# Performance work log

Hardware: AMD Instinct MI355X
Metric: run time of the kernel (lower is better)

Reference implementation:

```python
import jax, jax.numpy as jnp
import numpy as np

B, U, V, E, D, L4 = 64, 1024, 1024, 512, 640, 4 * 640


def setup_inputs() -> dict:
    key = jax.random.key(0)
    ks = jax.random.split(key, 9)
    return {
        "targets": jax.random.randint(ks[0], (B, U), 0, V),
        "target_lens": jax.random.randint(ks[1], (B,), 1, U + 1),
        "embed": jax.random.normal(ks[2], (V, E), dtype=jnp.float32) * 0.02,
        "W0": jax.random.normal(ks[3], (E, L4), dtype=jnp.float32) * 0.04,
        "U0": jax.random.normal(ks[4], (D, L4), dtype=jnp.float32) * 0.04,
        "b0": jnp.zeros((L4,), dtype=jnp.float32),
        "W1": jax.random.normal(ks[5], (D, L4), dtype=jnp.float32) * 0.04,
        "U1": jax.random.normal(ks[6], (D, L4), dtype=jnp.float32) * 0.04,
        "b1": jnp.zeros((L4,), dtype=jnp.float32),
    }


def _masked_lstm(x, mask, W, Uw, b):
    """Keras-semantics masked LSTM (i,f,g,o gate order). x:[B,T,in], mask:[B,T].
    Masked steps carry state/output forward (Keras RNN mask behavior)."""
    d = Uw.shape[0]
    xz = jnp.einsum('bti,ig->btg', x, W) + b  # precompute input projection [B,T,4D]

    def step(carry, inp):
        h, c = carry
        z_t, m = inp  # [B,4D], [B]
        z = z_t + h @ Uw
        i, f, g, o = jnp.split(z, 4, axis=-1)
        i = jax.nn.sigmoid(i)
        f = jax.nn.sigmoid(f)
        g = jnp.tanh(g)
        o = jax.nn.sigmoid(o)
        c_new = f * c + i * g
        h_new = o * jnp.tanh(c_new)
        m = m[:, None]
        h2 = jnp.where(m, h_new, h)
        c2 = jnp.where(m, c_new, c)
        return (h2, c2), h2

    h0 = jnp.zeros((x.shape[0], d), dtype=x.dtype)
    (_, _), ys = jax.lax.scan(step, (h0, h0), (xz.transpose(1, 0, 2), mask.T))
    return ys.transpose(1, 0, 2)  # [B,T,D]


def reference(targets, target_lens, embed, W0, U0, b0, W1, U1, b1):
    x = embed[targets]  # [B,U,E]
    mask = jnp.arange(targets.shape[1])[None, :] < target_lens[:, None]  # [B,U]
    x = _masked_lstm(x, mask, W0, U0, b0)
    x = _masked_lstm(x, mask, W1, U1, b1)
    return x
```

## Files before the change

kernel.cpp:

```cpp
#include <hip/hip_runtime.h>
#include <math.h>

#define B_   64
#define U_   1024
#define E_   512
#define D_   640
#define L4_  2560
#define TC   64
#define NCH  16
#define NBLK 160
#define SUBQ (NBLK / 8)

template <int MODE>
__global__ __launch_bounds__(256) void gemm_kernel(
    const float* __restrict__ A,
    const int*   __restrict__ targets,
    const float* __restrict__ Wm,
    const float* __restrict__ bias,
    float* __restrict__ xz,
    int K, int t0)
{
    const int tid = threadIdx.x;
    const int m0 = blockIdx.x * 128;
    const int n0 = blockIdx.y * 128;

    __shared__ float As[8][132];
    __shared__ float Bs[8][132];

    float acc[8][8];
#pragma unroll
    for (int i = 0; i < 8; ++i)
#pragma unroll
        for (int j = 0; j < 8; ++j) acc[i][j] = 0.f;

    const float* a_ptr;
    int a_ml = 0, a_kq = 0, a_k = 0;
    if (MODE == 0) {
        a_ml = tid & 127;
        a_kq = (tid >> 7) * 4;
        int m  = m0 + a_ml;
        int b  = m & 63;
        int tl = m >> 6;
        int idx = targets[b * U_ + t0 + tl];
        a_ptr = A + (size_t)idx * E_ + a_kq;
    } else {
        a_k  = tid >> 5;
        a_ml = (tid & 31) * 4;
        int m  = m0 + a_ml;
        int b  = m & 63;
        int tl = m >> 6;
        a_ptr = A + (size_t)tl * (D_ * 64) + (size_t)a_k * 64 + b;
    }
    const int b_k  = tid >> 5;
    const int b_n4 = (tid & 31) * 4;

    const int tx = tid & 15;
    const int ty = tid >> 4;

    for (int k0 = 0; k0 < K; k0 += 8) {
        if (MODE == 0) {
            float4 av = *(const float4*)(a_ptr + k0);
            As[a_kq + 0][a_ml] = av.x;
            As[a_kq + 1][a_ml] = av.y;
            As[a_kq + 2][a_ml] = av.z;
            As[a_kq + 3][a_ml] = av.w;
        } else {
            float4 av = *(const float4*)(a_ptr + (size_t)k0 * 64);
            *(float4*)&As[a_k][a_ml] = av;
        }
        {
            float4 bv = *(const float4*)(Wm + (size_t)(k0 + b_k) * L4_ + n0 + b_n4);
            *(float4*)&Bs[b_k][b_n4] = bv;
        }
        __syncthreads();

#pragma unroll
        for (int k = 0; k < 8; ++k) {
            float af[8], bf[8];
            *(float4*)&af[0] = *(const float4*)&As[k][ty * 8];
            *(float4*)&af[4] = *(const float4*)&As[k][ty * 8 + 4];
            *(float4*)&bf[0] = *(const float4*)&Bs[k][tx * 8];
            *(float4*)&bf[4] = *(const float4*)&Bs[k][tx * 8 + 4];
#pragma unroll
            for (int i = 0; i < 8; ++i)
#pragma unroll
                for (int j = 0; j < 8; ++j) acc[i][j] += af[i] * bf[j];
        }
        __syncthreads();
    }

#pragma unroll
    for (int i = 0; i < 8; ++i) {
        int m  = m0 + ty * 8 + i;
        int tl = m >> 6;
        int b  = m & 63;
        float* outp = xz + (size_t)tl * (L4_ * 64) + b;
#pragma unroll
        for (int j = 0; j < 8; ++j) {
            int n = n0 + tx * 8 + j;
            outp[(size_t)n * 64] = acc[i][j] + bias[n];
        }
    }
}

__global__ __launch_bounds__(256) void prep_up_kernel(
    const float* __restrict__ U0w, const float* __restrict__ U1w,
    float* __restrict__ Up0, float* __restrict__ Up1)
{
    const int k = blockIdx.x;
    const float* Uw = blockIdx.y ? U1w : U0w;
    float*       Up = blockIdx.y ? Up1 : Up0;
    for (int d = threadIdx.x; d < D_; d += 256) {
        const int g  = d >> 2;
        const int dd = d & 3;
#pragma unroll
        for (int gate = 0; gate < 4; ++gate) {
            float v = Uw[(size_t)k * L4_ + gate * 640 + d];
            Up[((size_t)g * 640 + k) * 16 + dd * 4 + gate] = v;
        }
    }
}

__device__ __forceinline__ void stg_llc(float* p, float v) {
    __hip_atomic_store(p, v, __ATOMIC_RELAXED, __HIP_MEMORY_SCOPE_AGENT);
}

__device__ __forceinline__ void grid_barrier(unsigned* bar, unsigned done)
{
    asm volatile("s_waitcnt vmcnt(0)" ::: "memory");
    __syncthreads();
    if (threadIdx.x == 0) {
        unsigned* sub    = bar + ((blockIdx.x & 7) << 5);
        unsigned* master = bar + (8 << 5);
        unsigned a = __hip_atomic_fetch_add(sub, 1u, __ATOMIC_RELAXED, __HIP_MEMORY_SCOPE_AGENT);
        if (a == done * SUBQ - 1u)
            __hip_atomic_fetch_add(master, 1u, __ATOMIC_RELAXED, __HIP_MEMORY_SCOPE_AGENT);
        const unsigned tgt = done * 8u;
        while (__hip_atomic_load(master, __ATOMIC_RELAXED, __HIP_MEMORY_SCOPE_AGENT) < tgt)
            __builtin_amdgcn_s_sleep(1);
    }
    __syncthreads();
}

__global__ __launch_bounds__(512) void lstm_seq_kernel(
    const float* __restrict__ xz,
    const float* __restrict__ Upg,
    const float* __restrict__ hinit,
    float* __restrict__ c_st,
    const int* __restrict__ lens,
    float* __restrict__ hc_out,
    int t0,
    unsigned* __restrict__ bar,
    unsigned bar_base)
{
    const int tid  = threadIdx.x;
    const int d0   = blockIdx.x * 4;
    const int ks   = tid >> 6;
    const int kbeg = ks * 80;
    const int lane   = tid & 63;
    const int n_grp  = lane >> 4;
    const int n_base = n_grp * 4;
    const int b0     = (lane & 15) * 4;

    __shared__ float U_lds[640 * 16];
    __shared__ float red[128][64];

    {
        const float4* upg = (const float4*)(Upg + (size_t)blockIdx.x * (640 * 16));
        float4* udst = (float4*)U_lds;
#pragma unroll
        for (int it = 0; it < 5; ++it)
            udst[it * 512 + tid] = upg[it * 512 + tid];
    }

    const bool epi = tid < 256;
    const int ed = d0 + ((tid >> 6) & 3);
    const int eb = tid & 63;
    float c_reg = 0.f;
    int   len_b = 0;
    if (epi) {
        c_reg = c_st[ed * 64 + eb];
        len_b = lens[eb];
    }

    __syncthreads();

    float acc[16];
    float HA[16], HB[16], HC[16];
    float UA[16], UB[16], UC[16];

#define HLOAD(HH)                                                           \
    _Pragma("unroll")                                                       \
    for (int j = 0; j < 4; ++j)                                             \
        *(float4*)&HH[j * 4] = *(const float4*)(hrun + j * 64);             \
    hrun += 256;

#define ULOAD(UU)                                                           \
    _Pragma("unroll")                                                       \
    for (int j = 0; j < 4; ++j)                                             \
        *(float4*)&UU[j * 4] = *(const float4*)(urun + j * 16);             \
    urun += 64;

#define FMAG(HH, UU)                                                        \
    _Pragma("unroll")                                                       \
    for (int j = 0; j < 4; ++j)                                             \
        _Pragma("unroll")                                                   \
        for (int i = 0; i < 4; ++i)                                         \
            _Pragma("unroll")                                               \
            for (int q = 0; q < 4; ++q)                                     \
                acc[i * 4 + q] += UU[j * 4 + i] * HH[j * 4 + q];

#pragma unroll 1
    for (int tl = 0; tl < TC; ++tl) {
        const int t = t0 + tl;
        const float* hprev = (tl == 0) ? hinit
                           : hc_out + (size_t)(tl - 1) * (D_ * 64);
        float*       hcur  = hc_out + (size_t)tl * (D_ * 64);

        float xzv[4];
        float hp_epi = 0.f;
        if (epi) {
            const float* xzp = xz + (size_t)tl * (L4_ * 64) + eb;
#pragma unroll
            for (int g = 0; g < 4; ++g)
                xzv[g] = xzp[(size_t)(ed + 640 * g) * 64];
            hp_epi = hprev[ed * 64 + eb];
        }

#pragma unroll
        for (int i = 0; i < 16; ++i) acc[i] = 0.f;

        const float* hrun = hprev + (size_t)kbeg * 64 + b0;
        const float* urun = &U_lds[(size_t)kbeg * 16 + n_base];

        HLOAD(HA) ULOAD(UA)
        HLOAD(HB) ULOAD(UB)
        HLOAD(HC) ULOAD(UC)
#pragma unroll 1
        for (int t3 = 0; t3 < 5; ++t3) {
            FMAG(HA, UA) HLOAD(HA) ULOAD(UA)
            FMAG(HB, UB) HLOAD(HB) ULOAD(UB)
            FMAG(HC, UC) HLOAD(HC) ULOAD(UC)
        }
        FMAG(HA, UA) HLOAD(HA) ULOAD(UA)
        FMAG(HB, UB) HLOAD(HB) ULOAD(UB)
        FMAG(HC, UC)
        FMAG(HA, UA)
        FMAG(HB, UB)

        {
            const int colw = b0 ^ (n_grp << 2);
#pragma unroll
            for (int i = 0; i < 4; ++i)
                *(float4*)&red[((n_base + i) << 3) | ks][colw] = *(float4*)&acc[i * 4];
        }
        __syncthreads();

        if (epi) {
            const int dd = (tid >> 6) & 3;
            const int colr = eb ^ (dd << 2);
            float z[4];
#pragma unroll
            for (int g = 0; g < 4; ++g) {
                const int r = ((dd * 4 + g) << 3);
                float s = 0.f;
#pragma unroll
                for (int kk = 0; kk < 8; ++kk) s += red[r + kk][colr];
                z[g] = s + xzv[g];
            }
            float ig = 1.f / (1.f + __expf(-z[0]));
            float fg = 1.f / (1.f + __expf(-z[1]));
            float gg = tanhf(z[2]);
            float og = 1.f / (1.f + __expf(-z[3]));
            float c_new = fg * c_reg + ig * gg;
            float h_new = og * tanhf(c_new);
            bool msk = t < len_b;
            float h_out = msk ? h_new : hp_epi;
            c_reg = msk ? c_new : c_reg;
            stg_llc(hcur + ed * 64 + eb, h_out);
        }

        if (tl != TC - 1)
            grid_barrier(bar, bar_base + (unsigned)tl + 1u);
    }
    if (epi) c_st[ed * 64 + eb] = c_reg;
#undef HLOAD
#undef ULOAD
#undef FMAG
}

__global__ __launch_bounds__(256) void transpose_kernel(
    const float* __restrict__ h1c, float* __restrict__ out, int t0)
{
    const int tl   = blockIdx.x;
    const int dblk = blockIdx.y;
    __shared__ float tile[64][65];

    const int r  = threadIdx.x >> 2;
    const int cq = threadIdx.x & 3;

    const float* src = h1c + (size_t)tl * (D_ * 64) + (size_t)(dblk * 64 + r) * 64 + cq * 16;
#pragma unroll
    for (int j = 0; j < 4; ++j) {
        float4 v = *(const float4*)(src + j * 4);
        tile[r][cq * 16 + j * 4 + 0] = v.x;
        tile[r][cq * 16 + j * 4 + 1] = v.y;
        tile[r][cq * 16 + j * 4 + 2] = v.z;
        tile[r][cq * 16 + j * 4 + 3] = v.w;
    }
    __syncthreads();

    float* dst = out + (size_t)r * (U_ * D_) + (size_t)(t0 + tl) * D_ + dblk * 64 + cq * 16;
#pragma unroll
    for (int j = 0; j < 4; ++j) {
        float4 w;
        w.x = tile[cq * 16 + j * 4 + 0][r];
        w.y = tile[cq * 16 + j * 4 + 1][r];
        w.z = tile[cq * 16 + j * 4 + 2][r];
        w.w = tile[cq * 16 + j * 4 + 3][r];
        *(float4*)(dst + j * 4) = w;
    }
}

extern "C" void kernel_launch(void* const* d_in, const int* in_sizes, int n_in,
                              void* d_out, int out_size, void* d_ws, size_t ws_size,
                              hipStream_t stream)
{
    const int*   targets = (const int*)d_in[0];
    const int*   lens    = (const int*)d_in[1];
    const float* embed   = (const float*)d_in[2];
    const float* W0      = (const float*)d_in[3];
    const float* U0      = (const float*)d_in[4];
    const float* b0      = (const float*)d_in[5];
    const float* W1      = (const float*)d_in[6];
    const float* U1      = (const float*)d_in[7];
    const float* b1      = (const float*)d_in[8];
    float* out = (float*)d_out;
    float* ws  = (float*)d_ws;

    float* xz  = ws;
    float* h0c = xz  + (size_t)TC * L4_ * 64;
    float* h1c = h0c + (size_t)TC * D_ * 64;
    float* st  = h1c + (size_t)TC * D_ * 64;
    float* hzero = st;
    float* c0  = st + 2 * 40960;
    float* c1  = st + 5 * 40960;
    unsigned* bar = (unsigned*)(st + 6 * 40960);
    float* Up0 = st + 6 * 40960 + 512;
    float* Up1 = Up0 + (size_t)D_ * L4_;

    hipMemsetAsync(st, 0, (size_t)6 * 40960 * sizeof(float) + 2048, stream);

    prep_up_kernel<<<dim3(D_, 2), dim3(256), 0, stream>>>(U0, U1, Up0, Up1);

    const dim3 gemm_grid(TC * 64 / 128, L4_ / 128);
    const dim3 blk(256);
    const dim3 blk_seq(512);

    unsigned launch_idx = 0;
    for (int ch = 0; ch < NCH; ++ch) {
        const int t0 = ch * TC;
        const float* hinit0 = (ch == 0) ? hzero : h0c + (size_t)(TC - 1) * (D_ * 64);
        const float* hinit1 = (ch == 0) ? hzero : h1c + (size_t)(TC - 1) * (D_ * 64);

        gemm_kernel<0><<<gemm_grid, blk, 0, stream>>>(embed, targets, W0, b0, xz, E_, t0);

        lstm_seq_kernel<<<dim3(NBLK), blk_seq, 0, stream>>>(
            xz, Up0, hinit0, c0, lens, h0c, t0, bar, launch_idx * 63u);
        ++launch_idx;

        gemm_kernel<1><<<gemm_grid, blk, 0, stream>>>(h0c, targets, W1, b1, xz, D_, t0);

        lstm_seq_kernel<<<dim3(NBLK), blk_seq, 0, stream>>>(
            xz, Up1, hinit1, c1, lens, h1c, t0, bar, launch_idx * 63u);
        ++launch_idx;

        transpose_kernel<<<dim3(TC, 10), blk, 0, stream>>>(h1c, out, t0);
    }
}
```

Before: 21.02 ms.

## Replace grid-wide barrier with per-group arrival counters and fine-grained waits

The full grid barrier after each timestep is replaced by eight group counters (20 blocks each). Each block bumps its group's counter after writing h. Each wave waits only on the group that produced the 80-row slice of h it reads. The previous-step h for the masked carry is also kept in a register instead of being reloaded from global memory. This cuts barrier latency and lets blocks start as soon as their inputs are ready, but it relies on relaxed atomics and a compiler-only fence for memory ordering.

```diff
diff --git a/kernel.cpp b/kernel.cpp
--- a/kernel.cpp
+++ b/kernel.cpp
@@ -9,7 +9,7 @@
 #define TC   64
 #define NCH  16
 #define NBLK 160
-#define SUBQ (NBLK / 8)
+#define GRPB 20
 
 template <int MODE>
 __global__ __launch_bounds__(256) void gemm_kernel(
@@ -125,21 +125,11 @@
     __hip_atomic_store(p, v, __ATOMIC_RELAXED, __HIP_MEMORY_SCOPE_AGENT);
 }
 
-__device__ __forceinline__ void grid_barrier(unsigned* bar, unsigned done)
-{
-    asm volatile("s_waitcnt vmcnt(0)" ::: "memory");
-    __syncthreads();
-    if (threadIdx.x == 0) {
-        unsigned* sub    = bar + ((blockIdx.x & 7) << 5);
-        unsigned* master = bar + (8 << 5);
-        unsigned a = __hip_atomic_fetch_add(sub, 1u, __ATOMIC_RELAXED, __HIP_MEMORY_SCOPE_AGENT);
-        if (a == done * SUBQ - 1u)
-            __hip_atomic_fetch_add(master, 1u, __ATOMIC_RELAXED, __HIP_MEMORY_SCOPE_AGENT);
-        const unsigned tgt = done * 8u;
-        while (__hip_atomic_load(master, __ATOMIC_RELAXED, __HIP_MEMORY_SCOPE_AGENT) < tgt)
-            __builtin_amdgcn_s_sleep(1);
-    }
-    __syncthreads();
+__device__ __forceinline__ void wait_group(const unsigned* arr, int g, unsigned tgt)
+{
+    while (__hip_atomic_load(arr + (g << 5), __ATOMIC_RELAXED, __HIP_MEMORY_SCOPE_AGENT) < tgt)
+        __builtin_amdgcn_s_sleep(1);
+    asm volatile("" ::: "memory");
 }
 
 __global__ __launch_bounds__(512) void lstm_seq_kernel(
@@ -150,13 +140,14 @@
     const int* __restrict__ lens,
     float* __restrict__ hc_out,
     int t0,
-    unsigned* __restrict__ bar,
-    unsigned bar_base)
+    unsigned* __restrict__ arr,
+    unsigned arr_base)
 {
     const int tid  = threadIdx.x;
     const int d0   = blockIdx.x * 4;
     const int ks   = tid >> 6;
     const int kbeg = ks * 80;
+    const int my_grp = blockIdx.x / GRPB;
     const int lane   = tid & 63;
     const int n_grp  = lane >> 4;
     const int n_base = n_grp * 4;
@@ -176,11 +167,12 @@
     const bool epi = tid < 256;
     const int ed = d0 + ((tid >> 6) & 3);
     const int eb = tid & 63;
-    float c_reg = 0.f;
+    float c_reg = 0.f, hpe = 0.f;
     int   len_b = 0;
     if (epi) {
         c_reg = c_st[ed * 64 + eb];
         len_b = lens[eb];
+        hpe   = hinit[ed * 64 + eb];
     }
 
     __syncthreads();
@@ -218,14 +210,15 @@
         float*       hcur  = hc_out + (size_t)tl * (D_ * 64);
 
         float xzv[4];
-        float hp_epi = 0.f;
         if (epi) {
             const float* xzp = xz + (size_t)tl * (L4_ * 64) + eb;
 #pragma unroll
             for (int g = 0; g < 4; ++g)
                 xzv[g] = xzp[(size_t)(ed + 640 * g) * 64];
-            hp_epi = hprev[ed * 64 + eb];
-        }
+        }
+
+        if (tl != 0)
+            wait_group(arr, ks, GRPB * (arr_base + (unsigned)tl));
 
 #pragma unroll
         for (int i = 0; i < 16; ++i) acc[i] = 0.f;
@@ -275,13 +268,19 @@
             float c_new = fg * c_reg + ig * gg;
             float h_new = og * tanhf(c_new);
             bool msk = t < len_b;
-            float h_out = msk ? h_new : hp_epi;
+            float h_out = msk ? h_new : hpe;
             c_reg = msk ? c_new : c_reg;
+            hpe   = h_out;
             stg_llc(hcur + ed * 64 + eb, h_out);
         }
 
-        if (tl != TC - 1)
-            grid_barrier(bar, bar_base + (unsigned)tl + 1u);
+        if (tl != TC - 1) {
+            asm volatile("s_waitcnt vmcnt(0)" ::: "memory");
+            __syncthreads();
+            if (tid == 0)
+                __hip_atomic_fetch_add(arr + (my_grp << 5), 1u,
+                                       __ATOMIC_RELAXED, __HIP_MEMORY_SCOPE_AGENT);
+        }
     }
     if (epi) c_st[ed * 64 + eb] = c_reg;
 #undef HLOAD
@@ -345,7 +344,7 @@
     float* hzero = st;
     float* c0  = st + 2 * 40960;
     float* c1  = st + 5 * 40960;
-    unsigned* bar = (unsigned*)(st + 6 * 40960);
+    unsigned* arr = (unsigned*)(st + 6 * 40960);
     float* Up0 = st + 6 * 40960 + 512;
     float* Up1 = Up0 + (size_t)D_ * L4_;
 
@@ -366,13 +365,13 @@
         gemm_kernel<0><<<gemm_grid, blk, 0, stream>>>(embed, targets, W0, b0, xz, E_, t0);
 
         lstm_seq_kernel<<<dim3(NBLK), blk_seq, 0, stream>>>(
-            xz, Up0, hinit0, c0, lens, h0c, t0, bar, launch_idx * 63u);
+            xz, Up0, hinit0, c0, lens, h0c, t0, arr, launch_idx * 63u);
         ++launch_idx;
 
         gemm_kernel<1><<<gemm_grid, blk, 0, stream>>>(h0c, targets, W1, b1, xz, D_, t0);
 
         lstm_seq_kernel<<<dim3(NBLK), blk_seq, 0, stream>>>(
-            xz, Up1, hinit1, c1, lens, h1c, t0, bar, launch_idx * 63u);
+            xz, Up1, hinit1, c1, lens, h1c, t0, arr, launch_idx * 63u);
         ++launch_idx;
 
         transpose_kernel<<<dim3(TC, 10), blk, 0, stream>>>(h1c, out, t0);
```

Result: slower. 23.79 ms (+13.2%).
